# Performance work log

Hardware: AMD Instinct MI355X
Metric: run time of the kernel (lower is better)

Reference implementation:

```python
import jax, jax.numpy as jnp
import numpy as np

# --- static config (mirrors args) ---
FOV = 79.0
RES = 5                      # map_resolution (cm/cell)
MAP_SIZE_CM = 4800           # map_size_cm // global_downscaling
VR = 100                     # vision_range (cells)
CAM_H_CM = 88.0              # camera_height * 100
CAT_THR, EXP_THR, MAP_THR = 5.0, 1.0, 1.0
MAX_H = 72                   # int(360 / 5)
MIN_H = -8                   # int(-40 / 5)
DEG = 57.29577951308232


def _splat(feat, coords, dims):
    """Trilinear splat (scatter-add) of feat [F,N] at coords [3,N] in [-1,1] into grid dims, then round."""
    F_, N = feat.shape
    Mtot = dims[0] * dims[1] * dims[2]
    pos = [coords[d] * dims[d] / 2.0 + dims[d] / 2.0 for d in range(3)]
    flo = [jnp.floor(p) for p in pos]
    grid = jnp.zeros((F_, Mtot), jnp.float32)
    for c0 in (0, 1):
        for c1 in (0, 1):
            for c2 in (0, 1):
                idx = jnp.zeros((N,), jnp.float32)
                wts = jnp.ones((N,), jnp.float32)
                for d, off in enumerate((c0, c1, c2)):
                    p = flo[d] + off
                    safe = ((p > 0) & (p < dims[d])).astype(jnp.float32)
                    wts = wts * (1.0 - jnp.abs(pos[d] - p)) * safe
                    idx = idx * dims[d] + p * safe
                grid = grid.at[:, idx.astype(jnp.int32)].add(feat * wts[None, :])
    return jnp.round(grid).reshape(F_, dims[0], dims[1], dims[2])


def _affine_grid(theta, H, W):
    # align_corners=True base grid; theta [2,3] -> grid [H,W,2] (x,y)
    gx, gy = jnp.meshgrid(jnp.linspace(-1.0, 1.0, W), jnp.linspace(-1.0, 1.0, H))
    base = jnp.stack([gx, gy, jnp.ones_like(gx)], -1)  # [H,W,3]
    return base @ theta.T


def _grid_sample(img, grid):
    # bilinear, zero padding, align_corners=True. img [C,H,W], grid [H,W,2]
    C, H, W = img.shape
    x = (grid[..., 0] + 1.0) * 0.5 * (W - 1)
    y = (grid[..., 1] + 1.0) * 0.5 * (H - 1)
    x0 = jnp.floor(x); y0 = jnp.floor(y)
    out = jnp.zeros_like(img)
    for yy, xx in ((y0, x0), (y0, x0 + 1), (y0 + 1, x0), (y0 + 1, x0 + 1)):
        w = (1.0 - jnp.abs(x - xx)) * (1.0 - jnp.abs(y - yy))
        inb = ((xx >= 0) & (xx <= W - 1) & (yy >= 0) & (yy <= H - 1)).astype(img.dtype)
        xi = jnp.clip(xx, 0, W - 1).astype(jnp.int32)
        yi = jnp.clip(yy, 0, H - 1).astype(jnp.int32)
        out = out + img[:, yi, xi] * (w * inb)[None]
    return out


def _forward(obs, pose_obs, maps_last, poses_last):
    bs, c, h, w = obs.shape
    depth = obs[0, 3]  # [h,w] in cm
    # camera matrix
    xc = (w - 1.0) / 2.0
    zc = (h - 1.0) / 2.0
    f = (w / 2.0) / np.tan(np.deg2rad(FOV / 2.0))
    gx = jnp.arange(w, dtype=jnp.float32)[None, :]
    gz = jnp.arange(h - 1, -1, -1, dtype=jnp.float32)[:, None]
    X = (gx - xc) * depth / f
    Z = (gz - zc) * depth / f
    # camera->agent (elevation 0 -> identity rot) then shift_loc (theta=pi/2 -> identity rot)
    X = X + VR * RES // 2
    Z = Z + CAM_H_CM
    zdim = MAX_H - MIN_H
    xs = (X / RES - VR // 2.0) / VR * 2.0
    ys = (depth / RES - VR // 2.0) / VR * 2.0
    zs = (Z / RES - (MAX_H + MIN_H) // 2.0) / zdim * 2.0
    N = h * w
    coords = jnp.stack([xs.reshape(N), ys.reshape(N), zs.reshape(N)], 0)  # [3,N]
    feat = jnp.concatenate([jnp.ones((1, N), jnp.float32), obs[0, 4:].reshape(c - 4, N)], 0)  # [F,N]
    voxels = _splat(feat, coords, (VR, VR, zdim))       # [F,VR,VR,Z]
    voxels = jnp.swapaxes(voxels, 1, 2)                  # .transpose(2,3)
    min_z = int(25 / RES - MIN_H)                        # 13
    max_z = int((CAM_H_CM + 1) / RES - MIN_H)            # 25
    ahp = voxels[..., min_z:max_z].sum(-1)               # [F,VR,VR]
    allp = voxels.sum(-1)
    fp_map = jnp.clip(ahp[0:1] / MAP_THR, 0.0, 1.0)
    fp_exp = jnp.clip(allp[0:1] / EXP_THR, 0.0, 1.0)
    M = MAP_SIZE_CM // RES
    x1 = M // 2 - VR // 2; x2 = x1 + VR
    y1 = M // 2; y2 = y1 + VR
    agent_view = jnp.zeros((c, M, M), jnp.float32)
    agent_view = agent_view.at[0:1, y1:y2, x1:x2].set(fp_map)
    agent_view = agent_view.at[1:2, y1:y2, x1:x2].set(fp_exp)
    agent_view = agent_view.at[4:, y1:y2, x1:x2].set(jnp.clip(ahp[1:] / CAT_THR, 0.0, 1.0))
    # pose integration (note: pose_pred aliases poses_last which is updated in-place in torch)
    th = poses_last[2] / DEG
    ny = poses_last[1] + pose_obs[0] * jnp.sin(th) + pose_obs[1] * jnp.cos(th)
    nx = poses_last[0] + pose_obs[0] * jnp.cos(th) - pose_obs[1] * jnp.sin(th)
    nt = poses_last[2] + pose_obs[2] * DEG
    nt = jnp.fmod(nt - 180.0, 360.0) + 180.0
    nt = jnp.fmod(nt + 180.0, 360.0) - 180.0
    current_pose = jnp.stack([nx, ny, nt])
    # spatial transform (st_pose is detached in torch)
    st = jax.lax.stop_gradient(current_pose)
    half = M // 2
    sx = -(st[0] * 100.0 / RES - half) / half
    sy = -(st[1] * 100.0 / RES - half) / half
    sth = (90.0 - st[2]) * np.pi / 180.0
    ct, sn = jnp.cos(sth), jnp.sin(sth)
    z = jnp.zeros(()); o = jnp.ones(())
    theta1 = jnp.stack([jnp.stack([ct, -sn, z]), jnp.stack([sn, ct, z])])
    theta2 = jnp.stack([jnp.stack([o, z, sx]), jnp.stack([z, o, sy])])
    rotated = _grid_sample(agent_view, _affine_grid(theta1, M, M))
    translated = _grid_sample(rotated, _affine_grid(theta2, M, M))
    # snap positive semantic cells (channels 4..7) to per-channel feature max
    ks = feat[1:5].max(axis=1)  # [4]
    sem = translated[4:8]
    translated = translated.at[4:8].set(jnp.where(sem > 0.0, ks[:, None, None], sem))
    map_pred = jnp.maximum(maps_last, translated)
    return fp_map, map_pred, current_pose, current_pose


def setup_inputs() -> dict:
    key = jax.random.key(0)
    k1, k2, k3, k4 = jax.random.split(key, 4)
    C = 9
    obs = jax.random.uniform(k1, (1, C, 480, 640), dtype=jnp.float32)
    obs = obs.at[:, 3].set(obs[:, 3] * 400.0 + 50.0)  # depth in cm, 50..450
    pose_obs = jax.random.uniform(k2, (3,), dtype=jnp.float32) * jnp.array([0.2, 0.2, 0.1], jnp.float32)
    maps_last = jax.random.uniform(k3, (C, 960, 960), dtype=jnp.float32)
    poses_last = jnp.array([24.0, 24.0, 0.0], jnp.float32) + jax.random.uniform(k4, (3,), dtype=jnp.float32) * jnp.array([2.0, 2.0, 30.0], jnp.float32)
    return {"obs": obs, "pose_obs": pose_obs, "maps_last": maps_last, "poses_last": poses_last}


def reference(obs, pose_obs, maps_last, poses_last):
    return _forward(obs, pose_obs, maps_last, poses_last)
```

## Files before the change

### kernel.cpp

```cpp
#include <hip/hip_runtime.h>
#include <math.h>

#define NPIX (480*640)
#define MDIM 960
#define MPIX (MDIM*MDIM)
#define PACK_M 307201u
#define CNT_STRIDE 32

#define SCAL_OFF 0
#define OFFS_OFF 80
#define SM_OFF   10084
#define PACK_OFF 80084
#define POS_OFF  387284
#define FEAT_OFF 1616084

#define OUT_FPMAP 0
#define OUT_MAP   10000
#define OUT_POSE  (10000 + 9*MPIX)

typedef float __attribute__((ext_vector_type(4))) f32x4;
__device__ __forceinline__ f32x4 ntload4(const float* p) {
    return __builtin_nontemporal_load((const f32x4*)p);
}
__device__ __forceinline__ void ntstore4(float* p, f32x4 v) {
    __builtin_nontemporal_store(v, (f32x4*)p);
}

__global__ __launch_bounds__(256) void count_kernel(const float* __restrict__ obs,
                                                    unsigned* __restrict__ cnt,
                                                    unsigned* __restrict__ pack,
                                                    float fcam) {
    int p = blockIdx.x*256 + threadIdx.x;
    int i = p / 640, j = p - i*640;
    float d = obs[3*NPIX + p];
    float X = ((float)j - 319.5f) * d / fcam + 250.0f;
    float Z = ((float)(479 - i) - 239.5f) * d / fcam + 88.0f;
    float xs = ((X/5.0f - 50.0f)/100.0f)*2.0f;
    float ys = ((d/5.0f - 50.0f)/100.0f)*2.0f;
    float zs = ((Z/5.0f - 32.0f)/80.0f)*2.0f;
    float pos0 = (xs*100.0f)/2.0f + 50.0f;
    float pos1 = (ys*100.0f)/2.0f + 50.0f;
    float pos2 = (zs*80.0f)/2.0f + 40.0f;
    int bx = (int)floorf(pos0), by = (int)floorf(pos1), bz = (int)floorf(pos2);
    unsigned pk = 0xFFFFFFFFu;
    if (bx >= 0 && bx <= 99 && by >= 0 && by <= 99 && bz >= 0 && bz <= 79) {
        unsigned b = (unsigned)(bx*100 + by);
        unsigned rank = atomicAdd(&cnt[b*CNT_STRIDE], 1u);
        pk = b * PACK_M + rank;
    }
    pack[p] = pk;
}

__global__ __launch_bounds__(256) void scan_pose_kernel(const unsigned* __restrict__ cnt,
                                                        unsigned* __restrict__ offs,
                                                        const float* pose_obs,
                                                        const float* poses_last,
                                                        float* scal, float* out_pose) {
    int tid = threadIdx.x;
    int lane = tid & 63, wave = tid >> 6;
    if (tid < 4) scal[16*(tid+1)] = 0.0f;
    unsigned lc[40];
    unsigned sum = 0;
    #pragma unroll
    for (int q = 0; q < 40; q++) {
        int idx = tid*40 + q;
        lc[q] = (idx < 10000) ? cnt[idx*CNT_STRIDE] : 0u;
        sum += lc[q];
    }
    unsigned incl = sum;
    #pragma unroll
    for (int off = 1; off < 64; off <<= 1) {
        unsigned u = (unsigned)__shfl_up((int)incl, off, 64);
        if (lane >= off) incl += u;
    }
    __shared__ unsigned wtot[4];
    if (lane == 63) wtot[wave] = incl;
    __syncthreads();
    unsigned pre = 0;
    for (int w = 0; w < wave; w++) pre += wtot[w];
    unsigned excl = pre + incl - sum;
    unsigned run = excl;
    #pragma unroll
    for (int q = 0; q < 40; q++) {
        int idx = tid*40 + q;
        if (idx < 10000) { offs[idx] = run; run += lc[q]; }
    }
    if (tid == 255) {
        offs[10000] = excl;
        const float DEGc = 57.29577951308232f;
        float th = poses_last[2] / DEGc;
        float s = sinf(th), c = cosf(th);
        float ny = poses_last[1] + pose_obs[0]*s + pose_obs[1]*c;
        float nx = poses_last[0] + pose_obs[0]*c - pose_obs[1]*s;
        float nt = poses_last[2] + pose_obs[2]*DEGc;
        nt = fmodf(nt - 180.0f, 360.0f) + 180.0f;
        nt = fmodf(nt + 180.0f, 360.0f) - 180.0f;
        out_pose[0] = nx; out_pose[1] = ny; out_pose[2] = nt;
        out_pose[3] = nx; out_pose[4] = ny; out_pose[5] = nt;
        float sx = -((nx*100.0f)/5.0f - 480.0f)/480.0f;
        float sy = -((ny*100.0f)/5.0f - 480.0f)/480.0f;
        float sth = ((90.0f - nt) * 3.14159265358979323846f) / 180.0f;
        scal[0] = cosf(sth);
        scal[1] = sinf(sth);
        scal[2] = sx;
        scal[3] = sy;
    }
}

__global__ __launch_bounds__(256) void scatter_kernel(const float* __restrict__ obs,
                                                      const unsigned* __restrict__ offs,
                                                      const unsigned* __restrict__ pack,
                                                      float4* __restrict__ pos,
                                                      float4* __restrict__ feat,
                                                      float* scal, float fcam) {
    int p = blockIdx.x*256 + threadIdx.x;
    int i = p / 640, j = p - i*640;
    unsigned pk = pack[p];
    float d  = obs[3*NPIX + p];
    float f1 = obs[4*NPIX + p];
    float f2 = obs[5*NPIX + p];
    float f3 = obs[6*NPIX + p];
    float f4 = obs[7*NPIX + p];
    float f5 = obs[8*NPIX + p];
    if (pk != 0xFFFFFFFFu) {
        unsigned b = pk / PACK_M;
        unsigned rank = pk - b * PACK_M;
        unsigned k = offs[b] + rank;
        float X = ((float)j - 319.5f) * d / fcam + 250.0f;
        float Z = ((float)(479 - i) - 239.5f) * d / fcam + 88.0f;
        float xs = ((X/5.0f - 50.0f)/100.0f)*2.0f;
        float ys = ((d/5.0f - 50.0f)/100.0f)*2.0f;
        float zs = ((Z/5.0f - 32.0f)/80.0f)*2.0f;
        float pos0 = (xs*100.0f)/2.0f + 50.0f;
        float pos1 = (ys*100.0f)/2.0f + 50.0f;
        float pos2 = (zs*80.0f)/2.0f + 40.0f;
        pos[k]  = make_float4(pos0, pos1, pos2, f1);
        feat[k] = make_float4(f2, f3, f4, f5);
    }
    float m0 = f1, m1 = f2, m2 = f3, m3 = f4;
    #pragma unroll
    for (int off = 32; off > 0; off >>= 1) {
        m0 = fmaxf(m0, __shfl_down(m0, off, 64));
        m1 = fmaxf(m1, __shfl_down(m1, off, 64));
        m2 = fmaxf(m2, __shfl_down(m2, off, 64));
        m3 = fmaxf(m3, __shfl_down(m3, off, 64));
    }
    __shared__ float red[4][4];
    int lane = threadIdx.x & 63, wave = threadIdx.x >> 6;
    if (lane == 0) {
        red[wave][0] = m0; red[wave][1] = m1; red[wave][2] = m2; red[wave][3] = m3;
    }
    __syncthreads();
    if (threadIdx.x < 4) {
        int c = threadIdx.x;
        float m = fmaxf(fmaxf(red[0][c], red[1][c]), fmaxf(red[2][c], red[3][c]));
        atomicMax((int*)&scal[16*(c+1)], __float_as_int(m));
    }
}

__global__ __launch_bounds__(256) void gather_kernel(const float4* __restrict__ pos,
                                                     const float4* __restrict__ feat,
                                                     const unsigned* __restrict__ offs,
                                                     float* __restrict__ sm,
                                                     float* __restrict__ out_fp) {
    int wave = threadIdx.x >> 6, lane = threadIdx.x & 63;
    int x = blockIdx.x % 100, y = blockIdx.x / 100;
    __shared__ float slabs[4][488];
    float* za = slabs[wave];
    for (int q = lane; q < 480; q += 64) za[q] = 0.0f;
    __syncthreads();
    if (x >= 1 && y >= 1) {
        int b0 = (x-1)*100 + (y-1);
        int b1 = x*100 + (y-1);
        unsigned s0 = offs[b0], e0 = offs[b0+2];
        unsigned s1 = offs[b1], e1 = offs[b1+2];
        unsigned n0 = e0 - s0, n = n0 + (e1 - s1);
        float xf = (float)x, yf = (float)y;
        for (unsigned idx = threadIdx.x; idx < n; idx += 256) {
            unsigned k = (idx < n0) ? (s0 + idx) : (s1 + idx - n0);
            float4 a  = pos[k];
            float4 q2 = feat[k];
            float w0 = 1.0f - fabsf(a.x - xf);
            float w1 = 1.0f - fabsf(a.y - yf);
            float w01 = w0 * w1;
            float bzf = floorf(a.z);
            #pragma unroll
            for (int c2 = 0; c2 <= 1; c2++) {
                float p2 = bzf + (float)c2;
                if (!(p2 > 0.0f && p2 < 80.0f)) continue;
                float w = w01 * (1.0f - fabsf(a.z - p2));
                int zi = (int)p2;
                int zb = zi * 6;
                atomicAdd(&za[zb + 0], w);
                if (zi >= 13 && zi < 25) {
                    atomicAdd(&za[zb + 1], w*a.w);
                    atomicAdd(&za[zb + 2], w*q2.x);
                    atomicAdd(&za[zb + 3], w*q2.y);
                    atomicAdd(&za[zb + 4], w*q2.z);
                    atomicAdd(&za[zb + 5], w*q2.w);
                }
            }
        }
    }
    __syncthreads();
    for (int q = threadIdx.x; q < 480; q += 256) {
        slabs[0][q] = slabs[0][q] + slabs[1][q] + slabs[2][q] + slabs[3][q];
    }
    __syncthreads();
    if (wave == 0) {
        int z = lane;
        float r0 = rintf(slabs[0][z*6 + 0]);
        float all0 = r0;
        if (lane < 16) all0 += rintf(slabs[0][(z + 64)*6 + 0]);
        bool inb = (z >= 13 && z < 25);
        float a0 = inb ? r0 : 0.0f;
        float a1 = inb ? rintf(slabs[0][z*6 + 1]) : 0.0f;
        float a2 = inb ? rintf(slabs[0][z*6 + 2]) : 0.0f;
        float a3 = inb ? rintf(slabs[0][z*6 + 3]) : 0.0f;
        float a4 = inb ? rintf(slabs[0][z*6 + 4]) : 0.0f;
        float a5 = inb ? rintf(slabs[0][z*6 + 5]) : 0.0f;
        #pragma unroll
        for (int off = 32; off > 0; off >>= 1) {
            all0 += __shfl_down(all0, off, 64);
            a0 += __shfl_down(a0, off, 64);
            a1 += __shfl_down(a1, off, 64);
            a2 += __shfl_down(a2, off, 64);
            a3 += __shfl_down(a3, off, 64);
            a4 += __shfl_down(a4, off, 64);
            a5 += __shfl_down(a5, off, 64);
        }
        if (lane == 0) {
            int t = y*100 + x;
            float fp = fminf(a0, 1.0f);
            float ex = fminf(all0, 1.0f);
            sm[0*10000 + t] = fp;
            sm[1*10000 + t] = ex;
            sm[2*10000 + t] = fminf(a1/5.0f, 1.0f);
            sm[3*10000 + t] = fminf(a2/5.0f, 1.0f);
            sm[4*10000 + t] = fminf(a3/5.0f, 1.0f);
            sm[5*10000 + t] = fminf(a4/5.0f, 1.0f);
            sm[6*10000 + t] = fminf(a5/5.0f, 1.0f);
            out_fp[t] = fp;
        }
    }
}

__device__ __forceinline__ void sample_agent(float gxv, float gyv,
                                             float ct, float sn,
                                             const float* __restrict__ sm,
                                             float rot[7]) {
    float u = ct*gxv - sn*gyv;
    float v = sn*gxv + ct*gyv;
    float xim = ((u + 1.0f)*0.5f)*959.0f;
    float yim = ((v + 1.0f)*0.5f)*959.0f;
    float x0 = floorf(xim), y0 = floorf(yim);
    #pragma unroll
    for (int ty = 0; ty <= 1; ty++) {
        float yy = y0 + (float)ty;
        if (yy < 480.0f || yy >= 580.0f) continue;
        float wy = 1.0f - fabsf(yim - yy);
        int yi = (int)yy - 480;
        #pragma unroll
        for (int tx = 0; tx <= 1; tx++) {
            float xx = x0 + (float)tx;
            if (xx < 430.0f || xx >= 530.0f) continue;
            float w = (1.0f - fabsf(xim - xx)) * wy;
            int o = yi*100 + ((int)xx - 430);
            #pragma unroll
            for (int k = 0; k < 7; k++) rot[k] += sm[k*10000 + o] * w;
        }
    }
}

__device__ __forceinline__ void pixel_ts(float xim, float yim, float ct, float sn,
                                         const float* __restrict__ sm, float ts[7]) {
    const float step = 2.0f/959.0f;
    float x0 = floorf(xim), y0 = floorf(yim);
    #pragma unroll
    for (int ty = 0; ty <= 1; ty++) {
        float yy = y0 + (float)ty;
        if (yy < 0.0f || yy > 959.0f) continue;
        float wy = 1.0f - fabsf(yim - yy);
        #pragma unroll
        for (int tx = 0; tx <= 1; tx++) {
            float xx = x0 + (float)tx;
            if (xx < 0.0f || xx > 959.0f) continue;
            float w = (1.0f - fabsf(xim - xx)) * wy;
            float rot[7] = {0,0,0,0,0,0,0};
            float gx1 = xx*step - 1.0f;
            float gy1 = yy*step - 1.0f;
            sample_agent(gx1, gy1, ct, sn, sm, rot);
            #pragma unroll
            for (int k = 0; k < 7; k++) ts[k] += rot[k]*w;
        }
    }
}

__global__ __launch_bounds__(256) void final_kernel(const float* __restrict__ maps_last,
                                                    const float* __restrict__ sm,
                                                    const float* __restrict__ scal,
                                                    float* __restrict__ out_map) {
    int g = blockIdx.x*256 + threadIdx.x;
    int p = g*4;
    int y = p / MDIM, xp = p - y*MDIM;
    float ct = scal[0], sn = scal[1], sx = scal[2], sy = scal[3];
    const float step = 2.0f/959.0f;
    float gyv = (float)y*step - 1.0f;
    float v = gyv + sy;
    float yim = ((v + 1.0f)*0.5f)*959.0f;
    float gyc = yim*step - 1.0f;
    float xims[4];
    bool act[4];
    bool any = false;
    #pragma unroll
    for (int q = 0; q < 4; q++) {
        float gxv = (float)(xp+q)*step - 1.0f;
        float u = gxv + sx;
        float xim = ((u + 1.0f)*0.5f)*959.0f;
        xims[q] = xim;
        float gxc = xim*step - 1.0f;
        float uc = ct*gxc - sn*gyc;
        float vc = sn*gxc + ct*gyc;
        float xc2 = ((uc + 1.0f)*0.5f)*959.0f;
        float yc2 = ((vc + 1.0f)*0.5f)*959.0f;
        bool a = (xc2 > 427.5f) && (xc2 < 531.5f) && (yc2 > 477.5f) && (yc2 < 581.5f);
        act[q] = a;
        any = any || a;
    }
    if (!any) {
        #pragma unroll
        for (int c = 0; c < 9; c++) {
            f32x4 ml = ntload4(maps_last + c*MPIX + p);
            f32x4 o;
            o.x = fmaxf(ml.x, 0.0f); o.y = fmaxf(ml.y, 0.0f);
            o.z = fmaxf(ml.z, 0.0f); o.w = fmaxf(ml.w, 0.0f);
            ntstore4(out_map + c*MPIX + p, o);
        }
        return;
    }
    float ks0 = scal[16], ks1 = scal[32], ks2 = scal[48], ks3 = scal[64];
    #pragma unroll
    for (int q = 0; q < 4; q++) {
        int o = p + q;
        float ts[7] = {0,0,0,0,0,0,0};
        if (act[q]) pixel_ts(xims[q], yim, ct, sn, sm, ts);
        float ml;
        ml = maps_last[0*MPIX + o]; out_map[0*MPIX + o] = fmaxf(ml, ts[0]);
        ml = maps_last[1*MPIX + o]; out_map[1*MPIX + o] = fmaxf(ml, ts[1]);
        ml = maps_last[2*MPIX + o]; out_map[2*MPIX + o] = fmaxf(ml, 0.0f);
        ml = maps_last[3*MPIX + o]; out_map[3*MPIX + o] = fmaxf(ml, 0.0f);
        float t4 = ts[2]; t4 = (t4 > 0.0f) ? ks0 : t4;
        ml = maps_last[4*MPIX + o]; out_map[4*MPIX + o] = fmaxf(ml, t4);
        float t5 = ts[3]; t5 = (t5 > 0.0f) ? ks1 : t5;
        ml = maps_last[5*MPIX + o]; out_map[5*MPIX + o] = fmaxf(ml, t5);
        float t6 = ts[4]; t6 = (t6 > 0.0f) ? ks2 : t6;
        ml = maps_last[6*MPIX + o]; out_map[6*MPIX + o] = fmaxf(ml, t6);
        float t7 = ts[5]; t7 = (t7 > 0.0f) ? ks3 : t7;
        ml = maps_last[7*MPIX + o]; out_map[7*MPIX + o] = fmaxf(ml, t7);
        ml = maps_last[8*MPIX + o]; out_map[8*MPIX + o] = fmaxf(ml, ts[6]);
    }
}

extern "C" void kernel_launch(void* const* d_in, const int* in_sizes, int n_in,
                              void* d_out, int out_size, void* d_ws, size_t ws_size,
                              hipStream_t stream) {
    const float* obs        = (const float*)d_in[0];
    const float* pose_obs   = (const float*)d_in[1];
    const float* maps_last  = (const float*)d_in[2];
    const float* poses_last = (const float*)d_in[3];
    float* out = (float*)d_out;

    unsigned* ws_u = (unsigned*)d_ws;
    float*    ws_f = (float*)d_ws;
    float*    scal = ws_f + SCAL_OFF;
    unsigned* offs = ws_u + OFFS_OFF;
    float*    sm   = ws_f + SM_OFF;
    unsigned* pack = ws_u + PACK_OFF;
    float4*   pos  = (float4*)(ws_f + POS_OFF);
    float4*   feat = (float4*)(ws_f + FEAT_OFF);
    unsigned* cnt  = ws_u + POS_OFF;

    hipMemsetAsync(ws_f + POS_OFF, 0, (size_t)10000 * CNT_STRIDE * 4u, stream);

    float fcam = (float)(320.0 / tan(39.5 * M_PI / 180.0));

    count_kernel<<<1200, 256, 0, stream>>>(obs, cnt, pack, fcam);
    scan_pose_kernel<<<1, 256, 0, stream>>>(cnt, offs, pose_obs, poses_last,
                                            scal, out + OUT_POSE);
    scatter_kernel<<<1200, 256, 0, stream>>>(obs, offs, pack, pos, feat, scal, fcam);
    gather_kernel<<<10000, 256, 0, stream>>>(pos, feat, offs, sm, out + OUT_FPMAP);
    final_kernel<<<900, 256, 0, stream>>>(maps_last, sm, scal, out + OUT_MAP);
}
```

Baseline: 223.1 us.

## Gather two map rows per block and split final kernel across channel groups

The gather kernel now has each block handle two adjacent y-cells for one x column. It reads the shared point range once and splats into two shared-memory slabs, which roughly halves redundant point loads and the block count. The final kernel is split into three channel groups, tripling the grid to 2700 blocks to raise memory-level parallelism on the 9-channel map copy. The cost is that each final_kernel thread recomputes the active-region test and any pixel_ts sampling three times, and the gather uses more shared memory per block.

```diff
diff --git a/kernel.cpp b/kernel.cpp
--- a/kernel.cpp
+++ b/kernel.cpp
@@ -164,61 +164,73 @@
                                                      float* __restrict__ sm,
                                                      float* __restrict__ out_fp) {
     int wave = threadIdx.x >> 6, lane = threadIdx.x & 63;
-    int x = blockIdx.x % 100, y = blockIdx.x / 100;
-    __shared__ float slabs[4][488];
+    int x  = blockIdx.x % 100;
+    int y0 = (blockIdx.x / 100) * 2;
+    __shared__ float slabs[4][2*488];
     float* za = slabs[wave];
-    for (int q = lane; q < 480; q += 64) za[q] = 0.0f;
+    for (int q = lane; q < 2*488; q += 64) za[q] = 0.0f;
     __syncthreads();
-    if (x >= 1 && y >= 1) {
-        int b0 = (x-1)*100 + (y-1);
-        int b1 = x*100 + (y-1);
-        unsigned s0 = offs[b0], e0 = offs[b0+2];
-        unsigned s1 = offs[b1], e1 = offs[b1+2];
+    if (x >= 1) {
+        int ylo  = (y0 > 0) ? (y0 - 1) : 0;
+        int yend = y0 + 2;
+        unsigned s0 = offs[(x-1)*100 + ylo];
+        unsigned e0 = offs[(x-1)*100 + yend];
+        unsigned s1 = offs[x*100 + ylo];
+        unsigned e1 = offs[x*100 + yend];
         unsigned n0 = e0 - s0, n = n0 + (e1 - s1);
-        float xf = (float)x, yf = (float)y;
+        float xf = (float)x;
         for (unsigned idx = threadIdx.x; idx < n; idx += 256) {
             unsigned k = (idx < n0) ? (s0 + idx) : (s1 + idx - n0);
             float4 a  = pos[k];
             float4 q2 = feat[k];
             float w0 = 1.0f - fabsf(a.x - xf);
-            float w1 = 1.0f - fabsf(a.y - yf);
-            float w01 = w0 * w1;
             float bzf = floorf(a.z);
+            int cy0i = (int)floorf(a.y);
             #pragma unroll
-            for (int c2 = 0; c2 <= 1; c2++) {
-                float p2 = bzf + (float)c2;
-                if (!(p2 > 0.0f && p2 < 80.0f)) continue;
-                float w = w01 * (1.0f - fabsf(a.z - p2));
-                int zi = (int)p2;
-                int zb = zi * 6;
-                atomicAdd(&za[zb + 0], w);
-                if (zi >= 13 && zi < 25) {
-                    atomicAdd(&za[zb + 1], w*a.w);
-                    atomicAdd(&za[zb + 2], w*q2.x);
-                    atomicAdd(&za[zb + 3], w*q2.y);
-                    atomicAdd(&za[zb + 4], w*q2.z);
-                    atomicAdd(&za[zb + 5], w*q2.w);
+            for (int tt = 0; tt <= 1; tt++) {
+                int cy = cy0i + tt;
+                if (cy <= 0 || cy >= 100) continue;
+                if (cy < y0 || cy > y0 + 1) continue;
+                float w1 = 1.0f - fabsf(a.y - (float)cy);
+                float w01 = w0 * w1;
+                float* zc = za + (cy - y0) * 488;
+                #pragma unroll
+                for (int c2 = 0; c2 <= 1; c2++) {
+                    float p2 = bzf + (float)c2;
+                    if (!(p2 > 0.0f && p2 < 80.0f)) continue;
+                    float w = w01 * (1.0f - fabsf(a.z - p2));
+                    int zi = (int)p2;
+                    int zb = zi * 6;
+                    atomicAdd(&zc[zb + 0], w);
+                    if (zi >= 13 && zi < 25) {
+                        atomicAdd(&zc[zb + 1], w*a.w);
+                        atomicAdd(&zc[zb + 2], w*q2.x);
+                        atomicAdd(&zc[zb + 3], w*q2.y);
+                        atomicAdd(&zc[zb + 4], w*q2.z);
+                        atomicAdd(&zc[zb + 5], w*q2.w);
+                    }
                 }
             }
         }
     }
     __syncthreads();
-    for (int q = threadIdx.x; q < 480; q += 256) {
+    for (int q = threadIdx.x; q < 2*488; q += 256) {
         slabs[0][q] = slabs[0][q] + slabs[1][q] + slabs[2][q] + slabs[3][q];
     }
     __syncthreads();
-    if (wave == 0) {
+    if (wave < 2) {
+        const float* zc = &slabs[0][wave*488];
         int z = lane;
-        float r0 = rintf(slabs[0][z*6 + 0]);
+        float r0 = rintf(zc[z*6 + 0]);
         float all0 = r0;
-        if (lane < 16) all0 += rintf(slabs[0][(z + 64)*6 + 0]);
+        if (lane < 16) all0 += rintf(zc[(z + 64)*6 + 0]);
         bool inb = (z >= 13 && z < 25);
         float a0 = inb ? r0 : 0.0f;
-        float a1 = inb ? rintf(slabs[0][z*6 + 1]) : 0.0f;
-        float a2 = inb ? rintf(slabs[0][z*6 + 2]) : 0.0f;
-        float a3 = inb ? rintf(slabs[0][z*6 + 3]) : 0.0f;
-        float a4 = inb ? rintf(slabs[0][z*6 + 4]) : 0.0f;
-        float a5 = inb ? rintf(slabs[0][z*6 + 5]) : 0.0f;
+        float a1 = inb ? rintf(zc[z*6 + 1]) : 0.0f;
+        float a2 = inb ? rintf(zc[z*6 + 2]) : 0.0f;
+        float a3 = inb ? rintf(zc[z*6 + 3]) : 0.0f;
+        float a4 = inb ? rintf(zc[z*6 + 4]) : 0.0f;
+        float a5 = inb ? rintf(zc[z*6 + 5]) : 0.0f;
         #pragma unroll
         for (int off = 32; off > 0; off >>= 1) {
             all0 += __shfl_down(all0, off, 64);
@@ -230,7 +242,7 @@
             a5 += __shfl_down(a5, off, 64);
         }
         if (lane == 0) {
-            int t = y*100 + x;
+            int t = (y0 + wave)*100 + x;
             float fp = fminf(a0, 1.0f);
             float ex = fminf(all0, 1.0f);
             sm[0*10000 + t] = fp;
@@ -300,9 +312,12 @@
                                                     const float* __restrict__ sm,
                                                     const float* __restrict__ scal,
                                                     float* __restrict__ out_map) {
-    int g = blockIdx.x*256 + threadIdx.x;
+    int part = blockIdx.x / 900;
+    int bb   = blockIdx.x - part*900;
+    int g = bb*256 + threadIdx.x;
     int p = g*4;
     int y = p / MDIM, xp = p - y*MDIM;
+    int c0 = part*3;
     float ct = scal[0], sn = scal[1], sx = scal[2], sy = scal[3];
     const float step = 2.0f/959.0f;
     float gyv = (float)y*step - 1.0f;
@@ -329,7 +344,7 @@
     }
     if (!any) {
         #pragma unroll
-        for (int c = 0; c < 9; c++) {
+        for (int c = c0; c < c0+3; c++) {
             f32x4 ml = ntload4(maps_last + c*MPIX + p);
             f32x4 o;
             o.x = fmaxf(ml.x, 0.0f); o.y = fmaxf(ml.y, 0.0f);
@@ -338,26 +353,23 @@
         }
         return;
     }
-    float ks0 = scal[16], ks1 = scal[32], ks2 = scal[48], ks3 = scal[64];
+    float ks[4] = {scal[16], scal[32], scal[48], scal[64]};
     #pragma unroll
     for (int q = 0; q < 4; q++) {
         int o = p + q;
         float ts[7] = {0,0,0,0,0,0,0};
         if (act[q]) pixel_ts(xims[q], yim, ct, sn, sm, ts);
-        float ml;
-        ml = maps_last[0*MPIX + o]; out_map[0*MPIX + o] = fmaxf(ml, ts[0]);
-        ml = maps_last[1*MPIX + o]; out_map[1*MPIX + o] = fmaxf(ml, ts[1]);
-        ml = maps_last[2*MPIX + o]; out_map[2*MPIX + o] = fmaxf(ml, 0.0f);
-        ml = maps_last[3*MPIX + o]; out_map[3*MPIX + o] = fmaxf(ml, 0.0f);
-        float t4 = ts[2]; t4 = (t4 > 0.0f) ? ks0 : t4;
-        ml = maps_last[4*MPIX + o]; out_map[4*MPIX + o] = fmaxf(ml, t4);
-        float t5 = ts[3]; t5 = (t5 > 0.0f) ? ks1 : t5;
-        ml = maps_last[5*MPIX + o]; out_map[5*MPIX + o] = fmaxf(ml, t5);
-        float t6 = ts[4]; t6 = (t6 > 0.0f) ? ks2 : t6;
-        ml = maps_last[6*MPIX + o]; out_map[6*MPIX + o] = fmaxf(ml, t6);
-        float t7 = ts[5]; t7 = (t7 > 0.0f) ? ks3 : t7;
-        ml = maps_last[7*MPIX + o]; out_map[7*MPIX + o] = fmaxf(ml, t7);
-        ml = maps_last[8*MPIX + o]; out_map[8*MPIX + o] = fmaxf(ml, ts[6]);
+        #pragma unroll
+        for (int c = c0; c < c0+3; c++) {
+            float ml = maps_last[c*MPIX + o];
+            float tv;
+            if (c == 0) tv = ts[0];
+            else if (c == 1) tv = ts[1];
+            else if (c == 2 || c == 3) tv = 0.0f;
+            else if (c == 8) tv = ts[6];
+            else { float t = ts[c-2]; tv = (t > 0.0f) ? ks[c-4] : t; }
+            out_map[c*MPIX + o] = fmaxf(ml, tv);
+        }
     }
 }
 
@@ -388,6 +400,6 @@
     scan_pose_kernel<<<1, 256, 0, stream>>>(cnt, offs, pose_obs, poses_last,
                                             scal, out + OUT_POSE);
     scatter_kernel<<<1200, 256, 0, stream>>>(obs, offs, pack, pos, feat, scal, fcam);
-    gather_kernel<<<10000, 256, 0, stream>>>(pos, feat, offs, sm, out + OUT_FPMAP);
-    final_kernel<<<900, 256, 0, stream>>>(maps_last, sm, scal, out + OUT_MAP);
-}
+    gather_kernel<<<5000, 256, 0, stream>>>(pos, feat, offs, sm, out + OUT_FPMAP);
+    final_kernel<<<2700, 256, 0, stream>>>(maps_last, sm, scal, out + OUT_MAP);
+}
```

Measured after the change: 228.6 us. 1.02x slower.
